# Optimization experiments

Measured on AMD Instinct MI355X. Metric: run time of the kernel, lower is better.

## Reference

```python
import jax, jax.numpy as jnp
import numpy as np

B, N, FEA = 4, 200000, 9
G = 32                      # per-axis index range used for voxel keys
NUM_SEG = B * G * G * G     # 131072 = max possible unique voxels (static)
OUT_DIM, COMPRE = 256, 16
BN_EPS = 1e-5

def _glorot(k, shape):
    lim = float(np.sqrt(6.0 / (shape[0] + shape[1])))
    return jax.random.uniform(k, shape, jnp.float32, -lim, lim)

def setup_inputs() -> dict:
    key = jax.random.key(0)
    ks = jax.random.split(key, 16)
    inp = {
        "pt_fea": jax.random.normal(ks[0], (B, N, FEA), jnp.float32),
        "xy_ind": jax.random.randint(ks[1], (B, N, 3), 0, G, dtype=jnp.int32),
    }
    dims = [FEA, 64, 128, 256, OUT_DIM]
    bn_dims = [FEA, 64, 128, 256]
    for i, d in enumerate(bn_dims):
        inp[f"bn{i}_g"] = jnp.ones((d,), jnp.float32)
        inp[f"bn{i}_b"] = jnp.zeros((d,), jnp.float32)
        inp[f"bn{i}_m"] = jax.random.normal(ks[2 + i], (d,), jnp.float32) * 0.1
        inp[f"bn{i}_v"] = jnp.ones((d,), jnp.float32)
    for i in range(4):
        inp[f"w{i+1}"] = _glorot(ks[6 + i], (dims[i], dims[i + 1]))
        inp[f"b{i+1}"] = jnp.zeros((dims[i + 1],), jnp.float32)
    inp["wc"] = _glorot(ks[10], (OUT_DIM, COMPRE))
    inp["bc"] = jnp.zeros((COMPRE,), jnp.float32)
    return inp

def _bn(x, g, b, m, v):
    return (x - m) * jax.lax.rsqrt(v + BN_EPS) * g + b

def reference(pt_fea, xy_ind, bn0_g, bn0_b, bn0_m, bn0_v,
              bn1_g, bn1_b, bn1_m, bn1_v, bn2_g, bn2_b, bn2_m, bn2_v,
              bn3_g, bn3_b, bn3_m, bn3_v,
              w1, b1, w2, b2, w3, b3, w4, b4, wc, bc):
    # flatten batched point clouds; build scalar voxel key = (batch, ix, iy, iz)
    b_idx = jnp.broadcast_to(jnp.arange(B, dtype=jnp.int32)[:, None], (B, N)).reshape(-1)
    ind = xy_ind.reshape(B * N, 3)
    keys = ((b_idx * G + ind[:, 0]) * G + ind[:, 1]) * G + ind[:, 2]  # [B*N]
    fea = pt_fea.reshape(B * N, FEA)

    # torch.unique(dim=0) equivalent: sorted unique keys + inverse map (static size)
    unq_keys, unq_inv = jnp.unique(keys, size=NUM_SEG, fill_value=-1, return_inverse=True)

    # torch_scatter.scatter_max over voxels
    pooled = jax.ops.segment_max(fea, unq_inv, num_segments=NUM_SEG)
    cnt = jax.ops.segment_sum(jnp.ones((B * N,), jnp.float32), unq_inv, num_segments=NUM_SEG)
    pooled = jnp.where(cnt[:, None] > 0, pooled, 0.0)  # neutralize empty padding slots (-inf)

    # PPmodel: BN -> Linear -> BN -> ReLU (x3) -> Linear (eval-mode BatchNorm)
    x = _bn(pooled, bn0_g, bn0_b, bn0_m, bn0_v)
    x = jax.nn.relu(_bn(x @ w1 + b1, bn1_g, bn1_b, bn1_m, bn1_v))
    x = jax.nn.relu(_bn(x @ w2 + b2, bn2_g, bn2_b, bn2_m, bn2_v))
    x = jax.nn.relu(_bn(x @ w3 + b3, bn3_g, bn3_b, bn3_m, bn3_v))
    x = x @ w4 + b4
    out = jax.nn.relu(x @ wc + bc)  # fea_compression

    # decode keys back to [num_vox, 4] int64 (batch, ix, iy, iz); padding rows = -1
    valid = unq_keys >= 0
    kk = jnp.where(valid, unq_keys, 0)
    unq = jnp.stack([kk // (G * G * G), (kk // (G * G)) % G, (kk // G) % G, kk % G], axis=1)
    unq = jnp.where(valid[:, None], unq, -1)
    return unq.astype(jnp.int64), out
```

## Files before the change

### kernel.cpp

```cpp
#include <hip/hip_runtime.h>

#define NPTS   800000
#define NPB    200000
#define NSEG   131072
#define OUT_OFF (NSEG*4)
#define BN_EPS 1e-5f
#define BCAP   2048
#define PLANE  (512*BCAP)

typedef __attribute__((ext_vector_type(8))) __bf16 bf16x8;
typedef __attribute__((ext_vector_type(4))) float  f32x4;

#define MFMA16 __builtin_amdgcn_mfma_f32_16x16x32_bf16

__device__ __forceinline__ unsigned short f2bf(float f) {
    unsigned u = __float_as_uint(f);
    u += 0x7fffu + ((u >> 16) & 1u);
    return (unsigned short)(u >> 16);
}
__device__ __forceinline__ unsigned enc16(unsigned short b) {
    return (b & 0x8000u) ? ((~(unsigned)b) & 0xFFFFu) : ((unsigned)b | 0x8000u);
}
__device__ __forceinline__ unsigned dec16(unsigned e) {
    return (e >= 0x8000u) ? (e & 0x7FFFu) : ((~e) & 0xFFFFu);
}

__global__ void k_fold(const float* __restrict__ g0, const float* __restrict__ be0,
                       const float* __restrict__ m0, const float* __restrict__ v0,
                       const float* __restrict__ g1, const float* __restrict__ be1,
                       const float* __restrict__ m1, const float* __restrict__ v1,
                       const float* __restrict__ g2, const float* __restrict__ be2,
                       const float* __restrict__ m2, const float* __restrict__ v2,
                       const float* __restrict__ g3, const float* __restrict__ be3,
                       const float* __restrict__ m3, const float* __restrict__ v3,
                       const float* __restrict__ w1, const float* __restrict__ b1,
                       const float* __restrict__ w2, const float* __restrict__ b2,
                       const float* __restrict__ w3, const float* __restrict__ b3,
                       const float* __restrict__ w4, const float* __restrict__ b4,
                       const float* __restrict__ wc, const float* __restrict__ bc,
                       unsigned short* __restrict__ WT1, float* __restrict__ c1,
                       unsigned short* __restrict__ WT2, float* __restrict__ c2,
                       unsigned short* __restrict__ WT3, float* __restrict__ c3,
                       unsigned short* __restrict__ WT4, float* __restrict__ c4,
                       unsigned* __restrict__ bucketFill) {
    __shared__ float swc[4096];
    int id = blockIdx.x * 256 + threadIdx.x;
    if (blockIdx.x >= 160 && blockIdx.x < 176) {
        for (int i = threadIdx.x; i < 4096; i += 256) swc[i] = wc[i];
        __syncthreads();
        int t = id - 40960; int j = t >> 8, k = t & 255;
        float acc = 0.f;
        const float4* w4r = reinterpret_cast<const float4*>(w4 + k*256);
        #pragma unroll 4
        for (int i4 = 0; i4 < 64; ++i4) {
            float4 w = w4r[i4];
            acc += w.x * swc[(i4*4+0)*16 + j] + w.y * swc[(i4*4+1)*16 + j]
                 + w.z * swc[(i4*4+2)*16 + j] + w.w * swc[(i4*4+3)*16 + j];
        }
        WT4[t] = f2bf(acc);
        return;
    }
    if (id < 32768) {
        int j = id >> 7, k = id & 127;
        float s = g3[j] * rsqrtf(v3[j] + BN_EPS);
        WT3[id] = f2bf(w3[k*256 + j] * s);
    } else if (id < 40960) {
        int t = id - 32768; int j = t >> 6, k = t & 63;
        float s = g2[j] * rsqrtf(v2[j] + BN_EPS);
        WT2[t] = f2bf(w2[k*128 + j] * s);
    } else if (id < 47104) {
        int t = id - 45056; int j = t >> 5, k = t & 31;
        float val = 0.f;
        if (k < 9) {
            float s0 = g0[k] * rsqrtf(v0[k] + BN_EPS);
            float s1 = g1[j] * rsqrtf(v1[j] + BN_EPS);
            val = s0 * w1[k*64 + j] * s1;
        }
        WT1[t] = f2bf(val);
    } else if (id < 47168) {
        int j = id - 47104;
        float s1 = g1[j] * rsqrtf(v1[j] + BN_EPS);
        float acc = b1[j];
        for (int k = 0; k < 9; ++k) {
            float s0 = g0[k] * rsqrtf(v0[k] + BN_EPS);
            float t0 = be0[k] - m0[k] * s0;
            acc += t0 * w1[k*64 + j];
        }
        c1[j] = (acc - m1[j]) * s1 + be1[j];
    } else if (id < 47296) {
        int j = id - 47168;
        float s = g2[j] * rsqrtf(v2[j] + BN_EPS);
        c2[j] = (b2[j] - m2[j]) * s + be2[j];
    } else if (id < 47552) {
        int j = id - 47296;
        float s = g3[j] * rsqrtf(v3[j] + BN_EPS);
        c3[j] = (b3[j] - m3[j]) * s + be3[j];
    } else if (id < 47568) {
        int j = id - 47552;
        float acc = bc[j];
        for (int i = 0; i < 256; ++i) acc += b4[i] * wc[i*16 + j];
        c4[j] = acc;
    } else if (id < 48080) {
        bucketFill[id - 47568] = 0u;
    }
}

__global__ void __launch_bounds__(512)
kC(const int* __restrict__ ind, const float* __restrict__ fea,
   unsigned* __restrict__ bucketFill, unsigned* __restrict__ bP) {
    __shared__ unsigned lh[128], gb[128];
    __shared__ unsigned stash[5][128*24];
    const int t = threadIdx.x;
    const int base = blockIdx.x * 1600;
    const int b0 = base / NPB;
    if (t < 128) lh[t] = 0u;
    __syncthreads();
    int loc[4]; unsigned slot[4]; unsigned pw[4][5];
    #pragma unroll
    for (int i = 0; i < 4; ++i) {
        int pl = i*512 + t;
        if (pl < 1600) {
            int p = base + pl;
            int ix = ind[p*3], iy = ind[p*3+1], iz = ind[p*3+2];
            loc[i] = ix*4 + (iy >> 3);
            unsigned v = (unsigned)((iy & 7)*32 + iz);
            const float* fp = fea + (size_t)p*9;
            float4 q0 = *reinterpret_cast<const float4*>(fp);
            float4 q1 = *reinterpret_cast<const float4*>(fp + 4);
            float  f8 = fp[8];
            unsigned e0 = enc16(f2bf(q0.x)), e1 = enc16(f2bf(q0.y));
            unsigned e2 = enc16(f2bf(q0.z)), e3 = enc16(f2bf(q0.w));
            unsigned e4 = enc16(f2bf(q1.x)), e5 = enc16(f2bf(q1.y));
            unsigned e6 = enc16(f2bf(q1.z)), e7 = enc16(f2bf(q1.w));
            unsigned e8 = enc16(f2bf(f8));
            pw[i][0] = (v << 16) | e0;
            pw[i][1] = e1 | (e2 << 16);
            pw[i][2] = e3 | (e4 << 16);
            pw[i][3] = e5 | (e6 << 16);
            pw[i][4] = e7 | (e8 << 16);
            slot[i] = atomicAdd(&lh[loc[i]], 1u);
            if (slot[i] < 24u) {
                #pragma unroll
                for (int w = 0; w < 5; ++w) stash[w][loc[i]*24 + slot[i]] = pw[i][w];
            }
        } else loc[i] = -1;
    }
    __syncthreads();
    if (t < 128 && lh[t] > 0u) gb[t] = atomicAdd(&bucketFill[b0*128 + t], lh[t]);
    __syncthreads();
    for (int idx = t; idx < 128*24; idx += 512) {
        int s = idx / 24, e = idx - s*24;
        unsigned n = lh[s]; if (n > 24u) n = 24u;
        if ((unsigned)e < n) {
            unsigned pos = gb[s] + (unsigned)e;
            if (pos < BCAP) {
                size_t off = (size_t)(b0*128 + s)*BCAP + pos;
                #pragma unroll
                for (int w = 0; w < 5; ++w) bP[(size_t)w*PLANE + off] = stash[w][idx];
            }
        }
    }
    #pragma unroll
    for (int i = 0; i < 4; ++i) if (loc[i] >= 0 && slot[i] >= 24u) {
        unsigned pos = gb[loc[i]] + slot[i];
        if (pos < BCAP) {
            size_t off = (size_t)(b0*128 + loc[i])*BCAP + pos;
            #pragma unroll
            for (int w = 0; w < 5; ++w) bP[(size_t)w*PLANE + off] = pw[i][w];
        }
    }
}

__global__ void __launch_bounds__(1024)
kD(const unsigned* __restrict__ bucketFill, const unsigned* __restrict__ bP,
   unsigned* __restrict__ pooledB, unsigned long long* __restrict__ occW) {
    __shared__ unsigned enc[256*9];
    const int t = threadIdx.x, bkt = blockIdx.x;
    for (int i = t; i < 2304; i += 1024) enc[i] = 0u;
    __syncthreads();
    unsigned n = bucketFill[bkt]; if (n > BCAP) n = BCAP;
    for (unsigned j = t; j < n; j += 1024) {
        size_t off = (size_t)bkt*BCAP + j;
        unsigned w0 = bP[off];
        unsigned w1 = bP[PLANE + off];
        unsigned w2 = bP[2*(size_t)PLANE + off];
        unsigned w3 = bP[3*(size_t)PLANE + off];
        unsigned w4 = bP[4*(size_t)PLANE + off];
        unsigned* eb = enc + (w0 >> 16)*9;
        atomicMax(eb+0, w0 & 0xFFFFu);
        atomicMax(eb+1, w1 & 0xFFFFu); atomicMax(eb+2, w1 >> 16);
        atomicMax(eb+3, w2 & 0xFFFFu); atomicMax(eb+4, w2 >> 16);
        atomicMax(eb+5, w3 & 0xFFFFu); atomicMax(eb+6, w3 >> 16);
        atomicMax(eb+7, w4 & 0xFFFFu); atomicMax(eb+8, w4 >> 16);
    }
    __syncthreads();
    if (t < 256) {
        int occ = (enc[t*9] != 0u) ? 1 : 0;
        unsigned long long m = __ballot(occ);
        if ((t & 63) == 0) occW[bkt*4 + (t >> 6)] = m;
    }
    for (int e2 = t; e2 < 1152; e2 += 1024) {
        int ea = 2*e2, eb2 = ea + 1;
        int va = ea / 9, vb = eb2 / 9;
        unsigned da = enc[va*9] ? dec16(enc[ea])  : 0u;
        unsigned db = enc[vb*9] ? dec16(enc[eb2]) : 0u;
        pooledB[(size_t)bkt*1152 + e2] = da | (db << 16);
    }
}


__device__ __forceinline__ void store4(char* base, int r, int strideElems, int n, f32x4 acc) {
    union { __bf16 h[4]; uint2 u; } pk;
    #pragma unroll
    for (int i = 0; i < 4; ++i) pk.h[i] = (__bf16)fmaxf(acc[i], 0.f);
    int s = n >> 3;
    *reinterpret_cast<uint2*>(base + r*strideElems*2 + ((s ^ (r & 7)) << 4) + (n & 4)*2) = pk.u;
}

__global__ void __launch_bounds__(512, 2)
k_mlp(const unsigned* __restrict__ pooledB,
      const unsigned long long* __restrict__ occW,
      const unsigned short* __restrict__ WT1, const float* __restrict__ c1,
      const unsigned short* __restrict__ WT2, const float* __restrict__ c2,
      const unsigned short* __restrict__ WT3, const float* __restrict__ c3,
      const unsigned short* __restrict__ WT4, const float* __restrict__ c4,
      float* __restrict__ unqOut, float* __restrict__ outF) {
    __shared__ __align__(16) char lds[61440];
    char* Rin = lds;
    char* H1  = lds + 4096;
    char* H2  = lds + 12288;
    char* H3  = lds + 28672;
    const int tid = threadIdx.x;
    const int wv = tid >> 6, lane = tid & 63;
    const int r16 = lane & 15, kg = lane >> 4;

    for (int i = tid; i < 1024; i += 512) reinterpret_cast<unsigned*>(Rin)[i] = 0u;

    const int ft1 = wv & 3;
    bf16x8 a1 = *reinterpret_cast<const bf16x8*>(WT1 + (ft1*16 + r16)*32 + kg*8);
    f32x4 c1v = *reinterpret_cast<const f32x4*>(c1 + ft1*16 + kg*4);
    bf16x8 a2[2];
    #pragma unroll
    for (int ks = 0; ks < 2; ++ks)
        a2[ks] = *reinterpret_cast<const bf16x8*>(WT2 + (wv*16 + r16)*64 + ks*32 + kg*8);
    f32x4 c2v = *reinterpret_cast<const f32x4*>(c2 + wv*16 + kg*4);
    bf16x8 a3[2][4]; f32x4 c3v[2];
    #pragma unroll
    for (int u = 0; u < 2; ++u) {
        int ft = wv*2 + u;
        #pragma unroll
        for (int ks = 0; ks < 4; ++ks)
            a3[u][ks] = *reinterpret_cast<const bf16x8*>(WT3 + (ft*16 + r16)*128 + ks*32 + kg*8);
        c3v[u] = *reinterpret_cast<const f32x4*>(c3 + ft*16 + kg*4);
    }
    bf16x8 a4[8]; f32x4 c4v;
    if (wv < 4) {
        #pragma unroll
        for (int ks = 0; ks < 8; ++ks)
            a4[ks] = *reinterpret_cast<const bf16x8*>(WT4 + r16*256 + ks*32 + kg*8);
        c4v = *reinterpret_cast<const f32x4*>(c4 + kg*4);
    }

    unsigned* sS  = reinterpret_cast<unsigned*>(H3);
    unsigned* wbS = reinterpret_cast<unsigned*>(H3 + 2048);
    unsigned pc0 = (unsigned)__popcll(occW[tid*4+0]);
    unsigned pc1 = (unsigned)__popcll(occW[tid*4+1]);
    unsigned pc2 = (unsigned)__popcll(occW[tid*4+2]);
    unsigned pc3 = (unsigned)__popcll(occW[tid*4+3]);
    unsigned psum = pc0 + pc1 + pc2 + pc3;
    sS[tid] = psum;
    __syncthreads();
    for (int off = 1; off < 512; off <<= 1) {
        unsigned add = (tid >= off) ? sS[tid-off] : 0u;
        __syncthreads();
        sS[tid] += add;
        __syncthreads();
    }
    unsigned ex = sS[tid] - psum;
    const unsigned tot = sS[511];
    #pragma unroll
    for (int k = 0; k < 8; ++k) {
        int tl = blockIdx.x + 256*k;
        if (tid == (tl >> 2)) {
            unsigned b = ex; int o = tl & 3;
            if (o > 0) b += pc0;
            if (o > 1) b += pc1;
            if (o > 2) b += pc2;
            wbS[k] = b;
        }
    }
    __syncthreads();
    unsigned wb[8];
    #pragma unroll
    for (int k = 0; k < 8; ++k) wb[k] = wbS[k];
    __syncthreads();

    int tile = blockIdx.x;
    unsigned pf;
    if (tid < 288) pf = pooledB[(size_t)tile*288 + tid];
    #pragma unroll 1
    for (int it = 0; it < 8; ++it) {
        if (tid < 288) {
            int ea = 2*tid, eb = ea + 1;
            int ra = ea / 9, ca = ea - ra*9;
            int rb = eb / 9, cb = eb - rb*9;
            *reinterpret_cast<unsigned short*>(Rin + ra*64 + (((ca>>3) ^ (ra&3))<<4) + (ca&7)*2)
                = (unsigned short)(pf & 0xFFFFu);
            *reinterpret_cast<unsigned short*>(Rin + rb*64 + (((cb>>3) ^ (rb&3))<<4) + (cb&7)*2)
                = (unsigned short)(pf >> 16);
        }
        unsigned long long w = occW[tile];
        unsigned base = wb[it];
        if (it < 7 && tid < 288) pf = pooledB[((size_t)tile + 256)*288 + tid];
        __syncthreads();
        {
            const int rtb = (wv >> 2) * 2;
            #pragma unroll
            for (int i = 0; i < 2; ++i) {
                int r = (rtb + i)*16 + r16;
                bf16x8 b = *reinterpret_cast<const bf16x8*>(Rin + r*64 + ((kg ^ (r&3))<<4));
                f32x4 acc = MFMA16(a1, b, c1v, 0, 0, 0);
                store4(H1, r, 64, ft1*16 + kg*4, acc);
            }
        }
        __syncthreads();
        #pragma unroll
        for (int rt = 0; rt < 4; ++rt) {
            int r = rt*16 + r16;
            bf16x8 b0 = *reinterpret_cast<const bf16x8*>(H1 + r*128 + ((kg ^ (r&7))<<4));
            bf16x8 b1 = *reinterpret_cast<const bf16x8*>(H1 + r*128 + (((4+kg) ^ (r&7))<<4));
            f32x4 acc = MFMA16(a2[0], b0, c2v, 0, 0, 0);
            acc = MFMA16(a2[1], b1, acc, 0, 0, 0);
            store4(H2, r, 128, wv*16 + kg*4, acc);
        }
        __syncthreads();
        #pragma unroll
        for (int rt = 0; rt < 4; ++rt) {
            int r = rt*16 + r16;
            bf16x8 b[4];
            #pragma unroll
            for (int ks = 0; ks < 4; ++ks)
                b[ks] = *reinterpret_cast<const bf16x8*>(H2 + r*256 + (((ks*4+kg) ^ (r&7))<<4));
            #pragma unroll
            for (int u = 0; u < 2; ++u) {
                f32x4 acc = c3v[u];
                #pragma unroll
                for (int ks = 0; ks < 4; ++ks)
                    acc = MFMA16(a3[u][ks], b[ks], acc, 0, 0, 0);
                store4(H3, r, 256, (wv*2+u)*16 + kg*4, acc);
            }
        }
        __syncthreads();
        if (wv < 4) {
            int r = wv*16 + r16;
            f32x4 acc = c4v;
            #pragma unroll
            for (int ks = 0; ks < 8; ++ks) {
                bf16x8 b = *reinterpret_cast<const bf16x8*>(H3 + r*512 + (((ks*4+kg) ^ (r&7))<<4));
                acc = MFMA16(a4[ks], b, acc, 0, 0, 0);
            }
            unsigned rdense = base + (unsigned)__popcll(w & ((1ull << r) - 1ull));
            unsigned rk = ((w >> r) & 1ull) ? rdense
                        : tot + (unsigned)(tile*64 + r) - rdense;
            float4 o;
            o.x = fmaxf(acc[0], 0.f); o.y = fmaxf(acc[1], 0.f);
            o.z = fmaxf(acc[2], 0.f); o.w = fmaxf(acc[3], 0.f);
            *reinterpret_cast<float4*>(outF + (size_t)rk*16 + kg*4) = o;
        } else if (wv == 4) {
            int r = lane, k = tile*64 + r;
            unsigned rdense = base + (unsigned)__popcll(w & ((1ull << r) - 1ull));
            if ((w >> r) & 1ull) {
                reinterpret_cast<float4*>(unqOut)[rdense] =
                    make_float4((float)(k >> 15), (float)((k >> 10) & 31),
                                (float)((k >> 5) & 31), (float)(k & 31));
            } else {
                unsigned er = tot + (unsigned)k - rdense;
                reinterpret_cast<float4*>(unqOut)[er] = make_float4(-1.f,-1.f,-1.f,-1.f);
            }
        }
        tile += 256;
    }
}

extern "C" void kernel_launch(void* const* d_in, const int* in_sizes, int n_in,
                              void* d_out, int out_size, void* d_ws, size_t ws_size,
                              hipStream_t stream) {
    const float* pt_fea = (const float*)d_in[0];
    const int*   xy_ind = (const int*)  d_in[1];
    const float* g0 = (const float*)d_in[2],  *be0 = (const float*)d_in[3];
    const float* m0 = (const float*)d_in[4],  *v0  = (const float*)d_in[5];
    const float* g1 = (const float*)d_in[6],  *be1 = (const float*)d_in[7];
    const float* m1 = (const float*)d_in[8],  *v1  = (const float*)d_in[9];
    const float* g2 = (const float*)d_in[10], *be2 = (const float*)d_in[11];
    const float* m2 = (const float*)d_in[12], *v2  = (const float*)d_in[13];
    const float* g3 = (const float*)d_in[14], *be3 = (const float*)d_in[15];
    const float* m3 = (const float*)d_in[16], *v3  = (const float*)d_in[17];
    const float* w1 = (const float*)d_in[18], *b1  = (const float*)d_in[19];
    const float* w2 = (const float*)d_in[20], *b2  = (const float*)d_in[21];
    const float* w3 = (const float*)d_in[22], *b3  = (const float*)d_in[23];
    const float* w4 = (const float*)d_in[24], *b4  = (const float*)d_in[25];
    const float* wc = (const float*)d_in[26], *bc  = (const float*)d_in[27];

    float* dout = (float*)d_out;

    unsigned* ws0 = (unsigned*)d_ws;
    unsigned long long* occW = (unsigned long long*)ws0;
    unsigned* bucketFill = ws0 + 4096;
    unsigned* pooledB    = ws0 + 4608;
    unsigned* bP         = pooledB + 512*1152;
    unsigned* wtBase     = bP + 5*(size_t)PLANE;
    unsigned short* WT1  = (unsigned short*)wtBase;
    unsigned short* WT2  = WT1 + 2048;
    unsigned short* WT3  = WT2 + 8192;
    unsigned short* WT4  = WT3 + 32768;
    float* c1 = (float*)(WT4 + 4096);
    float* c2 = c1 + 64;
    float* c3 = c2 + 128;
    float* c4 = c3 + 256;

    k_fold<<<188, 256, 0, stream>>>(g0,be0,m0,v0, g1,be1,m1,v1, g2,be2,m2,v2, g3,be3,m3,v3,
                                    w1,b1, w2,b2, w3,b3, w4,b4, wc,bc,
                                    WT1,c1, WT2,c2, WT3,c3, WT4,c4, bucketFill);
    kC<<<500, 512, 0, stream>>>(xy_ind, pt_fea, bucketFill, bP);
    kD<<<512, 1024, 0, stream>>>(bucketFill, bP, pooledB, occW);
    k_mlp<<<256, 512, 0, stream>>>(pooledB, occW,
                                   WT1,c1, WT2,c2, WT3,c3, WT4,c4, dout, dout + OUT_OFF);
}
```

Baseline: 60.46 us.

## Fuse weight-folding kernel into bucketing kernel and use wave-shuffle prefix scan

The separate weight/BN folding kernel is merged into the point bucketing kernel as extra blocks (500 bucketing blocks plus 93 folding blocks). The bucketFill zeroing moves to a hipMemsetAsync. This removes one kernel launch and lets the folding work overlap with bucketing. In the MLP kernel, the 512-thread shared-memory Hillis-Steele scan is replaced by a wave-level shuffle scan plus a small cross-wave sum, cutting many __syncthreads. The memset adds a separate stream operation, which may cost about as much as the launch it replaces.

```diff
diff --git a/kernel.cpp b/kernel.cpp
--- a/kernel.cpp
+++ b/kernel.cpp
@@ -25,92 +25,95 @@
     return (e >= 0x8000u) ? (e & 0x7FFFu) : ((~e) & 0xFFFFu);
 }
 
-__global__ void k_fold(const float* __restrict__ g0, const float* __restrict__ be0,
-                       const float* __restrict__ m0, const float* __restrict__ v0,
-                       const float* __restrict__ g1, const float* __restrict__ be1,
-                       const float* __restrict__ m1, const float* __restrict__ v1,
-                       const float* __restrict__ g2, const float* __restrict__ be2,
-                       const float* __restrict__ m2, const float* __restrict__ v2,
-                       const float* __restrict__ g3, const float* __restrict__ be3,
-                       const float* __restrict__ m3, const float* __restrict__ v3,
-                       const float* __restrict__ w1, const float* __restrict__ b1,
-                       const float* __restrict__ w2, const float* __restrict__ b2,
-                       const float* __restrict__ w3, const float* __restrict__ b3,
-                       const float* __restrict__ w4, const float* __restrict__ b4,
-                       const float* __restrict__ wc, const float* __restrict__ bc,
-                       unsigned short* __restrict__ WT1, float* __restrict__ c1,
-                       unsigned short* __restrict__ WT2, float* __restrict__ c2,
-                       unsigned short* __restrict__ WT3, float* __restrict__ c3,
-                       unsigned short* __restrict__ WT4, float* __restrict__ c4,
-                       unsigned* __restrict__ bucketFill) {
-    __shared__ float swc[4096];
-    int id = blockIdx.x * 256 + threadIdx.x;
-    if (blockIdx.x >= 160 && blockIdx.x < 176) {
-        for (int i = threadIdx.x; i < 4096; i += 256) swc[i] = wc[i];
-        __syncthreads();
-        int t = id - 40960; int j = t >> 8, k = t & 255;
-        float acc = 0.f;
-        const float4* w4r = reinterpret_cast<const float4*>(w4 + k*256);
-        #pragma unroll 4
-        for (int i4 = 0; i4 < 64; ++i4) {
-            float4 w = w4r[i4];
-            acc += w.x * swc[(i4*4+0)*16 + j] + w.y * swc[(i4*4+1)*16 + j]
-                 + w.z * swc[(i4*4+2)*16 + j] + w.w * swc[(i4*4+3)*16 + j];
-        }
-        WT4[t] = f2bf(acc);
+__global__ void __launch_bounds__(512)
+kCF(const int* __restrict__ ind, const float* __restrict__ fea,
+    const float* __restrict__ g0, const float* __restrict__ be0,
+    const float* __restrict__ m0, const float* __restrict__ v0,
+    const float* __restrict__ g1, const float* __restrict__ be1,
+    const float* __restrict__ m1, const float* __restrict__ v1,
+    const float* __restrict__ g2, const float* __restrict__ be2,
+    const float* __restrict__ m2, const float* __restrict__ v2,
+    const float* __restrict__ g3, const float* __restrict__ be3,
+    const float* __restrict__ m3, const float* __restrict__ v3,
+    const float* __restrict__ w1, const float* __restrict__ b1,
+    const float* __restrict__ w2, const float* __restrict__ b2,
+    const float* __restrict__ w3, const float* __restrict__ b3,
+    const float* __restrict__ w4, const float* __restrict__ b4,
+    const float* __restrict__ wc, const float* __restrict__ bc,
+    unsigned short* __restrict__ WT1, float* __restrict__ c1,
+    unsigned short* __restrict__ WT2, float* __restrict__ c2,
+    unsigned short* __restrict__ WT3, float* __restrict__ c3,
+    unsigned short* __restrict__ WT4, float* __restrict__ c4,
+    unsigned* __restrict__ bucketFill, unsigned* __restrict__ bP) {
+    __shared__ __align__(16) unsigned shm[15616];
+    const int t = threadIdx.x;
+
+    if (blockIdx.x >= 500) {
+        const int fid = blockIdx.x - 500;
+        const int id  = fid * 512 + t;
+        if (fid >= 80 && fid < 88) {
+            float* swc = reinterpret_cast<float*>(shm);
+            for (int i = t; i < 4096; i += 512) swc[i] = wc[i];
+            __syncthreads();
+            int q = id - 40960; int j = q >> 8, k = q & 255;
+            float acc = 0.f;
+            const float4* w4r = reinterpret_cast<const float4*>(w4 + k*256);
+            #pragma unroll 4
+            for (int i4 = 0; i4 < 64; ++i4) {
+                float4 w = w4r[i4];
+                acc += w.x * swc[(i4*4+0)*16 + j] + w.y * swc[(i4*4+1)*16 + j]
+                     + w.z * swc[(i4*4+2)*16 + j] + w.w * swc[(i4*4+3)*16 + j];
+            }
+            WT4[q] = f2bf(acc);
+            return;
+        }
+        if (id < 32768) {
+            int j = id >> 7, k = id & 127;
+            float s = g3[j] * rsqrtf(v3[j] + BN_EPS);
+            WT3[id] = f2bf(w3[k*256 + j] * s);
+        } else if (id < 40960) {
+            int q = id - 32768; int j = q >> 6, k = q & 63;
+            float s = g2[j] * rsqrtf(v2[j] + BN_EPS);
+            WT2[q] = f2bf(w2[k*128 + j] * s);
+        } else if (id >= 45056 && id < 47104) {
+            int q = id - 45056; int j = q >> 5, k = q & 31;
+            float val = 0.f;
+            if (k < 9) {
+                float s0 = g0[k] * rsqrtf(v0[k] + BN_EPS);
+                float s1 = g1[j] * rsqrtf(v1[j] + BN_EPS);
+                val = s0 * w1[k*64 + j] * s1;
+            }
+            WT1[q] = f2bf(val);
+        } else if (id >= 47104 && id < 47168) {
+            int j = id - 47104;
+            float s1 = g1[j] * rsqrtf(v1[j] + BN_EPS);
+            float acc = b1[j];
+            for (int k = 0; k < 9; ++k) {
+                float s0 = g0[k] * rsqrtf(v0[k] + BN_EPS);
+                float t0 = be0[k] - m0[k] * s0;
+                acc += t0 * w1[k*64 + j];
+            }
+            c1[j] = (acc - m1[j]) * s1 + be1[j];
+        } else if (id >= 47168 && id < 47296) {
+            int j = id - 47168;
+            float s = g2[j] * rsqrtf(v2[j] + BN_EPS);
+            c2[j] = (b2[j] - m2[j]) * s + be2[j];
+        } else if (id >= 47296 && id < 47552) {
+            int j = id - 47296;
+            float s = g3[j] * rsqrtf(v3[j] + BN_EPS);
+            c3[j] = (b3[j] - m3[j]) * s + be3[j];
+        } else if (id >= 47552 && id < 47568) {
+            int j = id - 47552;
+            float acc = bc[j];
+            for (int i = 0; i < 256; ++i) acc += b4[i] * wc[i*16 + j];
+            c4[j] = acc;
+        }
         return;
     }
-    if (id < 32768) {
-        int j = id >> 7, k = id & 127;
-        float s = g3[j] * rsqrtf(v3[j] + BN_EPS);
-        WT3[id] = f2bf(w3[k*256 + j] * s);
-    } else if (id < 40960) {
-        int t = id - 32768; int j = t >> 6, k = t & 63;
-        float s = g2[j] * rsqrtf(v2[j] + BN_EPS);
-        WT2[t] = f2bf(w2[k*128 + j] * s);
-    } else if (id < 47104) {
-        int t = id - 45056; int j = t >> 5, k = t & 31;
-        float val = 0.f;
-        if (k < 9) {
-            float s0 = g0[k] * rsqrtf(v0[k] + BN_EPS);
-            float s1 = g1[j] * rsqrtf(v1[j] + BN_EPS);
-            val = s0 * w1[k*64 + j] * s1;
-        }
-        WT1[t] = f2bf(val);
-    } else if (id < 47168) {
-        int j = id - 47104;
-        float s1 = g1[j] * rsqrtf(v1[j] + BN_EPS);
-        float acc = b1[j];
-        for (int k = 0; k < 9; ++k) {
-            float s0 = g0[k] * rsqrtf(v0[k] + BN_EPS);
-            float t0 = be0[k] - m0[k] * s0;
-            acc += t0 * w1[k*64 + j];
-        }
-        c1[j] = (acc - m1[j]) * s1 + be1[j];
-    } else if (id < 47296) {
-        int j = id - 47168;
-        float s = g2[j] * rsqrtf(v2[j] + BN_EPS);
-        c2[j] = (b2[j] - m2[j]) * s + be2[j];
-    } else if (id < 47552) {
-        int j = id - 47296;
-        float s = g3[j] * rsqrtf(v3[j] + BN_EPS);
-        c3[j] = (b3[j] - m3[j]) * s + be3[j];
-    } else if (id < 47568) {
-        int j = id - 47552;
-        float acc = bc[j];
-        for (int i = 0; i < 256; ++i) acc += b4[i] * wc[i*16 + j];
-        c4[j] = acc;
-    } else if (id < 48080) {
-        bucketFill[id - 47568] = 0u;
-    }
-}
-
-__global__ void __launch_bounds__(512)
-kC(const int* __restrict__ ind, const float* __restrict__ fea,
-   unsigned* __restrict__ bucketFill, unsigned* __restrict__ bP) {
-    __shared__ unsigned lh[128], gb[128];
-    __shared__ unsigned stash[5][128*24];
-    const int t = threadIdx.x;
+
+    unsigned* lh    = shm;
+    unsigned* gb    = shm + 128;
+    unsigned* stash = shm + 256;
     const int base = blockIdx.x * 1600;
     const int b0 = base / NPB;
     if (t < 128) lh[t] = 0u;
@@ -141,7 +144,7 @@
             slot[i] = atomicAdd(&lh[loc[i]], 1u);
             if (slot[i] < 24u) {
                 #pragma unroll
-                for (int w = 0; w < 5; ++w) stash[w][loc[i]*24 + slot[i]] = pw[i][w];
+                for (int w = 0; w < 5; ++w) stash[w*3072 + loc[i]*24 + slot[i]] = pw[i][w];
             }
         } else loc[i] = -1;
     }
@@ -156,7 +159,7 @@
             if (pos < BCAP) {
                 size_t off = (size_t)(b0*128 + s)*BCAP + pos;
                 #pragma unroll
-                for (int w = 0; w < 5; ++w) bP[(size_t)w*PLANE + off] = stash[w][idx];
+                for (int w = 0; w < 5; ++w) bP[(size_t)w*PLANE + off] = stash[w*3072 + idx];
             }
         }
     }
@@ -261,23 +264,30 @@
         c4v = *reinterpret_cast<const f32x4*>(c4 + kg*4);
     }
 
-    unsigned* sS  = reinterpret_cast<unsigned*>(H3);
-    unsigned* wbS = reinterpret_cast<unsigned*>(H3 + 2048);
+    unsigned* wtot = reinterpret_cast<unsigned*>(H3);
+    unsigned* wbS  = wtot + 8;
     unsigned pc0 = (unsigned)__popcll(occW[tid*4+0]);
     unsigned pc1 = (unsigned)__popcll(occW[tid*4+1]);
     unsigned pc2 = (unsigned)__popcll(occW[tid*4+2]);
     unsigned pc3 = (unsigned)__popcll(occW[tid*4+3]);
     unsigned psum = pc0 + pc1 + pc2 + pc3;
-    sS[tid] = psum;
-    __syncthreads();
-    for (int off = 1; off < 512; off <<= 1) {
-        unsigned add = (tid >= off) ? sS[tid-off] : 0u;
-        __syncthreads();
-        sS[tid] += add;
-        __syncthreads();
-    }
-    unsigned ex = sS[tid] - psum;
-    const unsigned tot = sS[511];
+    unsigned incl = psum;
+    #pragma unroll
+    for (int off = 1; off < 64; off <<= 1) {
+        unsigned up = __shfl_up(incl, off, 64);
+        if (lane >= off) incl += up;
+    }
+    if (lane == 63) wtot[wv] = incl;
+    __syncthreads();
+    unsigned prev = 0, tots = 0;
+    #pragma unroll
+    for (int wvi = 0; wvi < 8; ++wvi) {
+        unsigned v = wtot[wvi];
+        if (wvi < wv) prev += v;
+        tots += v;
+    }
+    const unsigned tot = tots;
+    unsigned ex = prev + incl - psum;
     #pragma unroll
     for (int k = 0; k < 8; ++k) {
         int tl = blockIdx.x + 256*k;
@@ -418,10 +428,12 @@
     float* c3 = c2 + 128;
     float* c4 = c3 + 256;
 
-    k_fold<<<188, 256, 0, stream>>>(g0,be0,m0,v0, g1,be1,m1,v1, g2,be2,m2,v2, g3,be3,m3,v3,
-                                    w1,b1, w2,b2, w3,b3, w4,b4, wc,bc,
-                                    WT1,c1, WT2,c2, WT3,c3, WT4,c4, bucketFill);
-    kC<<<500, 512, 0, stream>>>(xy_ind, pt_fea, bucketFill, bP);
+    hipMemsetAsync(bucketFill, 0, 512 * sizeof(unsigned), stream);
+    kCF<<<593, 512, 0, stream>>>(xy_ind, pt_fea,
+                                 g0,be0,m0,v0, g1,be1,m1,v1, g2,be2,m2,v2, g3,be3,m3,v3,
+                                 w1,b1, w2,b2, w3,b3, w4,b4, wc,bc,
+                                 WT1,c1, WT2,c2, WT3,c3, WT4,c4,
+                                 bucketFill, bP);
     kD<<<512, 1024, 0, stream>>>(bucketFill, bP, pooledB, occW);
     k_mlp<<<256, 512, 0, stream>>>(pooledB, occW,
                                    WT1,c1, WT2,c2, WT3,c3, WT4,c4, dout, dout + OUT_OFF);
```

After: 68.64 us. +13.5%, slower.
